# Performance work log

Measured on AMD Instinct MI355X. Metric: run time of the kernel, lower is better.

Reference implementation:

```python
import jax, jax.numpy as jnp
import numpy as np

N = 4096          # nodes
E = 131072        # edges (avg degree 32)
D_IN = 128        # node_dim
H = 256           # hidden_dim
HEADS = 8
DH = H // HEADS


def setup_inputs() -> dict:
    key = jax.random.key(0)
    ks = jax.random.split(key, 24)
    w = lambda k, shape: (jax.random.normal(k, shape, dtype=jnp.float32) * 0.05)
    inp = {
        "x": jax.random.normal(ks[0], (N, D_IN), dtype=jnp.float32),
        "edge_index": jax.random.randint(ks[1], (2, E), 0, N, dtype=jnp.int32),
        # GCN conv weights (PyG GCNConv: out = aggr(norm * x @ W) + b)
        "W1": w(ks[2], (D_IN, H)), "b1": jnp.zeros((H,), jnp.float32),
        "W2": w(ks[3], (H, H)),    "b2": jnp.zeros((H,), jnp.float32),
        "W3": w(ks[4], (H, H)),    "b3": jnp.zeros((H,), jnp.float32),
        # nn.MultiheadAttention params (torch layout: y = x @ W.T + b)
        "in_w": w(ks[5], (3 * H, H)), "in_b": jnp.zeros((3 * H,), jnp.float32),
        "out_w": w(ks[6], (H, H)),    "out_b": jnp.zeros((H,), jnp.float32),
        # failure_predictor MLP: H -> H/2 -> 3
        "fp1_w": w(ks[7], (H // 2, H)), "fp1_b": jnp.zeros((H // 2,), jnp.float32),
        "fp2_w": w(ks[8], (3, H // 2)), "fp2_b": jnp.zeros((3,), jnp.float32),
        # pattern_detector MLP: H -> H/2 -> 10
        "pd1_w": w(ks[9], (H // 2, H)),  "pd1_b": jnp.zeros((H // 2,), jnp.float32),
        "pd2_w": w(ks[10], (10, H // 2)), "pd2_b": jnp.zeros((10,), jnp.float32),
    }
    return inp


def gcn_conv(x, src, dst, W, b):
    """PyG GCNConv with self-loops and symmetric normalization."""
    h = x @ W                                   # [N, H]
    deg = jnp.zeros((N,), x.dtype).at[dst].add(1.0) + 1.0   # +1 for self-loop
    dinv = jax.lax.rsqrt(deg)
    norm = dinv[src] * dinv[dst]                # [E]
    agg = jnp.zeros_like(h).at[dst].add(h[src] * norm[:, None])
    agg = agg + h * (1.0 / deg)[:, None]        # self-loop term: deg^-1/2 * deg^-1/2
    return agg + b


def mha(h, in_w, in_b, out_w, out_b):
    qkv = h @ in_w.T + in_b                     # [N, 3H]
    q, k, v = jnp.split(qkv, 3, axis=-1)
    q = q.reshape(N, HEADS, DH).transpose(1, 0, 2)   # [h, N, dh]
    k = k.reshape(N, HEADS, DH).transpose(1, 0, 2)
    v = v.reshape(N, HEADS, DH).transpose(1, 0, 2)
    scores = jnp.einsum("hnd,hmd->hnm", q, k) / np.sqrt(DH)
    attn = jax.nn.softmax(scores, axis=-1)
    o = jnp.einsum("hnm,hmd->hnd", attn, v)          # [h, N, dh]
    o = o.transpose(1, 0, 2).reshape(N, H)
    return o @ out_w.T + out_b


def reference(x, edge_index, W1, b1, W2, b2, W3, b3, in_w, in_b, out_w, out_b,
              fp1_w, fp1_b, fp2_w, fp2_b, pd1_w, pd1_b, pd2_w, pd2_b):
    src, dst = edge_index[0], edge_index[1]
    h = jax.nn.relu(gcn_conv(x, src, dst, W1, b1))   # dropout is identity in eval
    h = jax.nn.relu(gcn_conv(h, src, dst, W2, b2))
    h = gcn_conv(h, src, dst, W3, b3)
    h = h + mha(h, in_w, in_b, out_w, out_b)
    risk = jax.nn.softmax(jax.nn.relu(h @ fp1_w.T + fp1_b) @ fp2_w.T + fp2_b, axis=-1)
    patterns = jax.nn.sigmoid(jax.nn.relu(h @ pd1_w.T + pd1_b) @ pd2_w.T + pd2_b)
    return risk, patterns
```

## Files before the change

### kernel.cpp

```cpp
#include <hip/hip_runtime.h>
#include <math.h>

static constexpr int NNODE = 4096;
static constexpr int HDIM  = 256;
static constexpr int DIN   = 128;
static constexpr int HEADS = 8;
static constexpr int SPLIT = 4;

using short8 = __attribute__((ext_vector_type(8))) short;
using f32x4  = __attribute__((ext_vector_type(4))) float;

__device__ inline unsigned short bfr(float x) {
    union { float f; unsigned u; } v; v.f = x;
    unsigned r = v.u + 0x7FFFu + ((v.u >> 16) & 1u);
    return (unsigned short)(r >> 16);
}
__device__ inline float bf2f(unsigned short u) {
    union { unsigned u; float f; } v; v.u = (unsigned)u << 16; return v.f;
}
__device__ inline unsigned cvt_pk_bf16(float lo, float hi) {
    unsigned r;
    asm("v_cvt_pk_bf16_f32 %0, %1, %2" : "=v"(r) : "v"(lo), "v"(hi));
    return r;
}
__device__ inline float ex2(float x) {
    float r;
    asm("v_exp_f32 %0, %1" : "=v"(r) : "v"(x));
    return r;
}

static constexpr float QSCALE_LOG2 = 0.25503527f;

__global__ __launch_bounds__(256) void k_scan_norm(const int* __restrict__ degi,
        int* __restrict__ off, int* __restrict__ cursor,
        float* __restrict__ dinv, float* __restrict__ invdeg) {
    __shared__ int partial[256];
    int t = threadIdx.x;
    int local[16];
    int s = 0;
    #pragma unroll
    for (int i = 0; i < 16; ++i) { local[i] = degi[t * 16 + i]; s += local[i]; }
    partial[t] = s;
    __syncthreads();
    #pragma unroll
    for (int d = 1; d < 256; d <<= 1) {
        int add = (t >= d) ? partial[t - d] : 0;
        __syncthreads();
        partial[t] += add;
        __syncthreads();
    }
    int b = partial[t] - s;
    #pragma unroll
    for (int i = 0; i < 16; ++i) {
        int n = t * 16 + i;
        off[n] = b; cursor[n] = b; b += local[i];
        float d = (float)local[i] + 1.0f;
        dinv[n]   = rsqrtf(d);
        invdeg[n] = 1.0f / d;
    }
}

__global__ void k_fill(const int* __restrict__ ei, int* __restrict__ cursor,
                       int* __restrict__ csr, int E) {
    int e = blockIdx.x * 256 + threadIdx.x;
    if (e < E) {
        int d = ei[E + e];
        int p = atomicAdd(&cursor[d], 1);
        csr[p] = ei[e];
    }
}

__global__ __launch_bounds__(256) void k_prep(
        const float* __restrict__ W1, const float* __restrict__ W2,
        const float* __restrict__ W3, const float* __restrict__ in_w,
        const float* __restrict__ outw, const float* __restrict__ fp1w,
        const float* __restrict__ pd1w, const float* __restrict__ fp1b,
        const float* __restrict__ pd1b, const float* __restrict__ x,
        const int* __restrict__ ei, int E, int* __restrict__ degi,
        unsigned short* __restrict__ W1t, unsigned short* __restrict__ W2t,
        unsigned short* __restrict__ W3t, unsigned short* __restrict__ in_wb,
        unsigned short* __restrict__ outwb, unsigned short* __restrict__ wcatb,
        float* __restrict__ bcat, unsigned short* __restrict__ xb) {
    int idx = blockIdx.x * 256 + threadIdx.x;
    if (idx < 32768) {
        int c = idx >> 7, k = idx & 127;
        W1t[idx] = bfr(W1[(size_t)k * 256 + c]);
    } else if (idx < 98304) {
        int j = idx - 32768; int c = j >> 8, k = j & 255;
        W2t[j] = bfr(W2[(size_t)k * 256 + c]);
    } else if (idx < 163840) {
        int j = idx - 98304; int c = j >> 8, k = j & 255;
        W3t[j] = bfr(W3[(size_t)k * 256 + c]);
    } else if (idx < 360448) {
        int j = idx - 163840;
        in_wb[j] = bfr(in_w[j]);
    } else if (idx < 425984) {
        int j = idx - 360448;
        outwb[j] = bfr(outw[j]);
    } else if (idx < 491520) {
        int j = idx - 425984;
        int row = j >> 8, k = j & 255;
        wcatb[j] = bfr(row < 128 ? fp1w[(size_t)row * 256 + k]
                                 : pd1w[(size_t)(row - 128) * 256 + k]);
        if (j < 256) bcat[j] = (j < 128) ? fp1b[j] : pd1b[j - 128];
    } else if (idx < 557056) {
        int i = (idx - 491520) * 8;
        float4 a = *(const float4*)&x[i];
        float4 b = *(const float4*)&x[i + 4];
        short8 o;
        o[0]=(short)bfr(a.x); o[1]=(short)bfr(a.y); o[2]=(short)bfr(a.z); o[3]=(short)bfr(a.w);
        o[4]=(short)bfr(b.x); o[5]=(short)bfr(b.y); o[6]=(short)bfr(b.z); o[7]=(short)bfr(b.w);
        *(short8*)&xb[i] = o;
    } else if (idx < 557056 + E) {
        atomicAdd(&degi[ei[E + (idx - 557056)]], 1);
    }
}

template<int K, int EPI, bool BIAS, bool ADD>
__global__ __launch_bounds__(256) void k_bgemm(
        const unsigned short* __restrict__ A, const unsigned short* __restrict__ B,
        const float* __restrict__ bias, const float* __restrict__ addsrc,
        void* __restrict__ P0, void* __restrict__ P1, void* __restrict__ P2,
        int Nout) {
    const int lane = threadIdx.x & 63, wave = threadIdx.x >> 6;
    const int ql = lane & 15, g = lane >> 4;
    const int m0w = blockIdx.y * 64 + wave * 16;
    const int n0 = blockIdx.x * 32;
    const unsigned short* ap = A + (size_t)(m0w + ql) * K + g * 8;
    const unsigned short* bp = B + (size_t)(n0 + ql) * K + g * 8;

    f32x4 acc[2] = {{0,0,0,0},{0,0,0,0}};
    #pragma unroll
    for (int k0 = 0; k0 < K; k0 += 32) {
        short8 a = *(const short8*)(ap + k0);
        #pragma unroll
        for (int nt = 0; nt < 2; ++nt) {
            short8 b = *(const short8*)(bp + (size_t)nt * 16 * K + k0);
            acc[nt] = __builtin_amdgcn_mfma_f32_16x16x32_bf16(a, b, acc[nt], 0, 0, 0);
        }
    }
    #pragma unroll
    for (int nt = 0; nt < 2; ++nt) {
        const int col = n0 + nt * 16 + ql;
        const float bv = BIAS ? bias[col] : 0.f;
        if (EPI == 2) {
            const int sec = col >> 8, cc = col & 255;
            const int head = cc >> 5, dh = cc & 31;
            if (sec == 2) {
                unsigned short* dst = (unsigned short*)P2
                    + ((size_t)head * 32 + dh) * NNODE + m0w + g * 4;
                uint2 pk;
                pk.x = cvt_pk_bf16(acc[nt][0] + bv, acc[nt][1] + bv);
                pk.y = cvt_pk_bf16(acc[nt][2] + bv, acc[nt][3] + bv);
                *(uint2*)dst = pk;
            } else {
                unsigned short* dst = (unsigned short*)(sec == 0 ? P0 : P1);
                const float sc = (sec == 0) ? QSCALE_LOG2 : 1.0f;
                #pragma unroll
                for (int i = 0; i < 4; ++i) {
                    int row = m0w + g * 4 + i;
                    dst[((size_t)head * NNODE + row) * 32 + dh] = bfr((acc[nt][i] + bv) * sc);
                }
            }
        } else if (EPI == 1) {
            unsigned short* Cb = (unsigned short*)P0;
            #pragma unroll
            for (int i = 0; i < 4; ++i) {
                int row = m0w + g * 4 + i;
                float v = acc[nt][i] + bv;
                if (ADD) v += addsrc[(size_t)row * Nout + col];
                Cb[(size_t)row * Nout + col] = bfr(v);
            }
        } else {
            float* Cf = (float*)P0;
            #pragma unroll
            for (int i = 0; i < 4; ++i) {
                int row = m0w + g * 4 + i;
                float v = acc[nt][i] + bv;
                if (ADD) v += addsrc[(size_t)row * Nout + col];
                Cf[(size_t)row * Nout + col] = v;
            }
        }
    }
}

__global__ __launch_bounds__(256) void k_bgemm_merge(
        const unsigned short* __restrict__ po, const float* __restrict__ pl,
        const unsigned short* __restrict__ B, const float* __restrict__ bias,
        const float* __restrict__ addsrc, unsigned short* __restrict__ Cb) {
    constexpr int K = HDIM;
    const int lane = threadIdx.x & 63, wave = threadIdx.x >> 6;
    const int ql = lane & 15, g = lane >> 4;
    const int m0w = blockIdx.y * 64 + wave * 16;
    const int n0 = blockIdx.x * 32;
    const int row = m0w + ql;
    const unsigned short* bp = B + (size_t)(n0 + ql) * K + g * 8;

    f32x4 acc[2] = {{0,0,0,0},{0,0,0,0}};
    #pragma unroll
    for (int k0 = 0; k0 < K; k0 += 32) {
        const int kidx = k0 + g * 8;
        const int hd = kidx >> 5, dh0 = kidx & 31;
        const size_t b4 = ((size_t)hd * NNODE + row) * SPLIT;
        float L = pl[b4] + pl[b4 + 1] + pl[b4 + 2] + pl[b4 + 3];
        float rcpL = 1.f / L;
        short8 p0 = *(const short8*)&po[(b4 + 0) * 32 + dh0];
        short8 p1 = *(const short8*)&po[(b4 + 1) * 32 + dh0];
        short8 p2 = *(const short8*)&po[(b4 + 2) * 32 + dh0];
        short8 p3 = *(const short8*)&po[(b4 + 3) * 32 + dh0];
        float vch[8];
        #pragma unroll
        for (int i = 0; i < 8; ++i) {
            vch[i] = (bf2f((unsigned short)p0[i]) + bf2f((unsigned short)p1[i])
                    + bf2f((unsigned short)p2[i]) + bf2f((unsigned short)p3[i])) * rcpL;
        }
        short8 a;
        #pragma unroll
        for (int i = 0; i < 4; ++i) {
            unsigned pk = cvt_pk_bf16(vch[2*i], vch[2*i+1]);
            a[2*i]   = (short)(pk & 0xFFFF);
            a[2*i+1] = (short)(pk >> 16);
        }
        #pragma unroll
        for (int nt = 0; nt < 2; ++nt) {
            short8 b = *(const short8*)(bp + (size_t)nt * 16 * K + k0);
            acc[nt] = __builtin_amdgcn_mfma_f32_16x16x32_bf16(a, b, acc[nt], 0, 0, 0);
        }
    }
    #pragma unroll
    for (int nt = 0; nt < 2; ++nt) {
        const int col = n0 + nt * 16 + ql;
        const float bv = bias[col];
        #pragma unroll
        for (int i = 0; i < 4; ++i) {
            int r = m0w + g * 4 + i;
            float v = acc[nt][i] + bv + addsrc[(size_t)r * HDIM + col];
            Cb[(size_t)r * HDIM + col] = bfr(v);
        }
    }
}

template<int MODE>
__global__ __launch_bounds__(256) void k_gather(const unsigned short* __restrict__ hW,
        const int* __restrict__ csr, const int* __restrict__ off,
        const int* __restrict__ degi, const float* __restrict__ dinv,
        const float* __restrict__ invdeg, const float* __restrict__ bias,
        float* __restrict__ aggf, unsigned short* __restrict__ aggb) {
    const int n = blockIdx.x;
    const int c = threadIdx.x;
    const int start = off[n];
    const int cnt = degi[n];
    __shared__ int   sidx[64];
    __shared__ float swht[64];
    float a0 = 0.f, a1 = 0.f, a2 = 0.f, a3 = 0.f;
    for (int k0 = 0; k0 < cnt; k0 += 64) {
        __syncthreads();
        if (c < 64 && k0 + c < cnt) {
            int s = csr[start + k0 + c];
            sidx[c] = s;
            swht[c] = dinv[s];
        }
        __syncthreads();
        int lim = min(64, cnt - k0);
        int k = 0;
        for (; k + 4 <= lim; k += 4) {
            a0 += bf2f(hW[(size_t)sidx[k+0] * HDIM + c]) * swht[k+0];
            a1 += bf2f(hW[(size_t)sidx[k+1] * HDIM + c]) * swht[k+1];
            a2 += bf2f(hW[(size_t)sidx[k+2] * HDIM + c]) * swht[k+2];
            a3 += bf2f(hW[(size_t)sidx[k+3] * HDIM + c]) * swht[k+3];
        }
        for (; k < lim; ++k)
            a0 += bf2f(hW[(size_t)sidx[k] * HDIM + c]) * swht[k];
    }
    float acc = (a0 + a1) + (a2 + a3);
    float val = acc * dinv[n] + bf2f(hW[(size_t)n * HDIM + c]) * invdeg[n] + bias[c];
    if (MODE == 0) {
        aggb[(size_t)n * HDIM + c] = bfr(fmaxf(val, 0.f));
    } else {
        aggf[(size_t)n * HDIM + c] = val;
        aggb[(size_t)n * HDIM + c] = bfr(val);
    }
}

__device__ inline void softmax_16q(f32x4 st[4], float& l,
        unsigned short* prow, int g) {
    float ll = 0.f;
    #pragma unroll
    for (int t = 0; t < 4; ++t) {
        float p0 = ex2(st[t][0]);
        float p1 = ex2(st[t][1]);
        float p2 = ex2(st[t][2]);
        float p3 = ex2(st[t][3]);
        ll += (p0 + p1) + (p2 + p3);
        uint2 w2; w2.x = cvt_pk_bf16(p0, p1); w2.y = cvt_pk_bf16(p2, p3);
        *(uint2*)&prow[t * 16 + g * 4] = w2;
    }
    ll += __shfl_xor(ll, 16);
    ll += __shfl_xor(ll, 32);
    l += ll;
}

__global__ __launch_bounds__(256, 4) void k_attn_mfma(const unsigned short* __restrict__ qh,
        const unsigned short* __restrict__ kh, const unsigned short* __restrict__ vt,
        unsigned short* __restrict__ po, float* __restrict__ pl) {
    const int bid = blockIdx.x;
    const int hd = bid & 7;
    const int z  = (bid >> 3) & (SPLIT - 1);
    const int qb = bid >> 5;
    const int tid = threadIdx.x;
    const int wave = tid >> 6, lane = tid & 63;
    const int ql = lane & 15, g = lane >> 4;

    __shared__ unsigned short Klds[2][64 * 40];
    __shared__ unsigned short Vt[2][32 * 72];
    __shared__ unsigned short Plds[4][16 * 72];

    const unsigned short* khh = kh + (size_t)hd * NNODE * 32;
    const unsigned short* vtt = vt + (size_t)hd * 32 * NNODE;
    const int row = qb * 64 + wave * 16 + ql;
    short8 qf = *(const short8*)(qh + ((size_t)hd * NNODE + row) * 32 + g * 8);

    f32x4 oa0 = {0,0,0,0}, oa1 = {0,0,0,0};
    float l = 0.f;

    const int skey = tid >> 2, skc = (tid & 3) * 8;
    const int sdh = tid >> 3, sch = (tid & 7) * 8;
    const unsigned short* ksrc = khh + (size_t)skey * 32 + skc;
    const unsigned short* vsrc = vtt + (size_t)sdh * NNODE + sch;
    unsigned short* prow = &Plds[wave][ql * 72];
    const int TPS = NNODE / 64 / SPLIT;
    const int t0 = z * TPS;

    {
        short8 kv = *(const short8*)(ksrc + (size_t)t0 * 64 * 32);
        short8 vv = *(const short8*)(vsrc + t0 * 64);
        *(short8*)&Klds[0][skey * 40 + skc] = kv;
        *(short8*)&Vt[0][sdh * 72 + sch] = vv;
    }
    __syncthreads();
    int cur = 0;

    for (int kt = t0; kt < t0 + TPS; ++kt) {
        short8 kv, vv;
        const bool pref = (kt + 1 < t0 + TPS);
        if (pref) {
            kv = *(const short8*)(ksrc + (size_t)(kt + 1) * 64 * 32);
            vv = *(const short8*)(vsrc + (kt + 1) * 64);
        }

        f32x4 st[4];
        __builtin_amdgcn_s_setprio(1);
        #pragma unroll
        for (int t = 0; t < 4; ++t) {
            short8 kf = *(const short8*)&Klds[cur][(t * 16 + ql) * 40 + g * 8];
            st[t] = __builtin_amdgcn_mfma_f32_16x16x32_bf16(kf, qf, (f32x4){0,0,0,0}, 0, 0, 0);
        }
        __builtin_amdgcn_s_setprio(0);

        softmax_16q(st, l, prow, g);

        if (pref) {
            *(short8*)&Klds[cur ^ 1][skey * 40 + skc] = kv;
            *(short8*)&Vt[cur ^ 1][sdh * 72 + sch] = vv;
        }

        __builtin_amdgcn_s_setprio(1);
        #pragma unroll
        for (int c = 0; c < 2; ++c) {
            short8 pf = *(const short8*)&prow[c * 32 + g * 8];
            short8 v0 = *(const short8*)&Vt[cur][ql * 72 + c * 32 + g * 8];
            short8 v1 = *(const short8*)&Vt[cur][(16 + ql) * 72 + c * 32 + g * 8];
            oa0 = __builtin_amdgcn_mfma_f32_16x16x32_bf16(v0, pf, oa0, 0, 0, 0);
            oa1 = __builtin_amdgcn_mfma_f32_16x16x32_bf16(v1, pf, oa1, 0, 0, 0);
        }
        __builtin_amdgcn_s_setprio(0);

        __syncthreads();
        cur ^= 1;
    }

    const size_t pidx = ((size_t)hd * NNODE + row) * SPLIT + z;
    unsigned short* pp = po + pidx * 32;
    uint2 r;
    r.x = cvt_pk_bf16(oa0[0], oa0[1]); r.y = cvt_pk_bf16(oa0[2], oa0[3]);
    *(uint2*)&pp[g * 4] = r;
    r.x = cvt_pk_bf16(oa1[0], oa1[1]); r.y = cvt_pk_bf16(oa1[2], oa1[3]);
    *(uint2*)&pp[16 + g * 4] = r;
    if (g == 0) pl[pidx] = l;
}

__global__ __launch_bounds__(256) void k_heads2(const float* __restrict__ th,
        const float* __restrict__ fp2w, const float* __restrict__ fp2b,
        const float* __restrict__ pd2w, const float* __restrict__ pd2b,
        float* __restrict__ out) {
    const int wave = threadIdx.x >> 6, lane = threadIdx.x & 63;
    const int n = blockIdx.x * 4 + wave;
    const int half = lane >> 5;
    const int li = lane & 31;
    float4 h4 = *(const float4*)&th[(size_t)n * HDIM + half * 128 + li * 4];
    h4.x = fmaxf(h4.x, 0.f); h4.y = fmaxf(h4.y, 0.f);
    h4.z = fmaxf(h4.z, 0.f); h4.w = fmaxf(h4.w, 0.f);
    float lf[3];
    float lp[10];
    #pragma unroll
    for (int j = 0; j < 10; ++j) {
        float partial = 0.f;
        if (half == 0) {
            if (j < 3) {
                float4 wv = *(const float4*)&fp2w[j * 128 + li * 4];
                partial = h4.x*wv.x + h4.y*wv.y + h4.z*wv.z + h4.w*wv.w;
            }
        } else {
            float4 wv = *(const float4*)&pd2w[j * 128 + li * 4];
            partial = h4.x*wv.x + h4.y*wv.y + h4.z*wv.z + h4.w*wv.w;
        }
        #pragma unroll
        for (int d = 1; d < 32; d <<= 1) partial += __shfl_xor(partial, d);
        if (j < 3) lf[j] = partial;
        lp[j] = partial;
    }
    if (lane == 0) {
        float l0 = lf[0] + fp2b[0], l1 = lf[1] + fp2b[1], l2 = lf[2] + fp2b[2];
        float mx = fmaxf(l0, fmaxf(l1, l2));
        float e0 = __expf(l0 - mx), e1 = __expf(l1 - mx), e2 = __expf(l2 - mx);
        float inv = 1.f / (e0 + e1 + e2);
        out[(size_t)n * 3 + 0] = e0 * inv;
        out[(size_t)n * 3 + 1] = e1 * inv;
        out[(size_t)n * 3 + 2] = e2 * inv;
    } else if (lane == 32) {
        #pragma unroll
        for (int j = 0; j < 10; ++j)
            out[(size_t)NNODE * 3 + (size_t)n * 10 + j] =
                1.f / (1.f + __expf(-(lp[j] + pd2b[j])));
    }
}

extern "C" void kernel_launch(void* const* d_in, const int* in_sizes, int n_in,
                              void* d_out, int out_size, void* d_ws, size_t ws_size,
                              hipStream_t stream) {
    const float* x    = (const float*)d_in[0];
    const int*   ei   = (const int*)  d_in[1];
    const float* W1   = (const float*)d_in[2];
    const float* b1   = (const float*)d_in[3];
    const float* W2   = (const float*)d_in[4];
    const float* b2   = (const float*)d_in[5];
    const float* W3   = (const float*)d_in[6];
    const float* b3   = (const float*)d_in[7];
    const float* in_w = (const float*)d_in[8];
    const float* in_b = (const float*)d_in[9];
    const float* outw = (const float*)d_in[10];
    const float* outb = (const float*)d_in[11];
    const float* fp1w = (const float*)d_in[12];
    const float* fp1b = (const float*)d_in[13];
    const float* fp2w = (const float*)d_in[14];
    const float* fp2b = (const float*)d_in[15];
    const float* pd1w = (const float*)d_in[16];
    const float* pd1b = (const float*)d_in[17];
    const float* pd2w = (const float*)d_in[18];
    const float* pd2b = (const float*)d_in[19];
    float* out = (float*)d_out;

    const int E = in_sizes[1] / 2;

    char* w = (char*)d_ws;
    auto alloc = [&](size_t bytes) {
        char* p = w; w += (bytes + 255) & ~(size_t)255; return p;
    };
    int*   degi   = (int*)alloc(NNODE * 4);
    int*   off    = (int*)alloc(NNODE * 4);
    int*   cursor = (int*)alloc(NNODE * 4);
    int*   csr    = (int*)alloc((size_t)E * 4);
    float* dinv   = (float*)alloc(NNODE * 4);
    float* invdeg = (float*)alloc(NNODE * 4);
    unsigned short* W1t   = (unsigned short*)alloc(256 * 128 * 2);
    unsigned short* W2t   = (unsigned short*)alloc(256 * 256 * 2);
    unsigned short* W3t   = (unsigned short*)alloc(256 * 256 * 2);
    unsigned short* in_wb = (unsigned short*)alloc(768 * 256 * 2);
    unsigned short* outwb = (unsigned short*)alloc(256 * 256 * 2);
    unsigned short* wcatb = (unsigned short*)alloc(256 * 256 * 2);
    float* bcat  = (float*)alloc(256 * 4);
    unsigned short* xb    = (unsigned short*)alloc((size_t)NNODE * DIN * 2);
    float* bufA  = (float*)alloc((size_t)NNODE * HDIM * 4);
    unsigned short* bufAb = (unsigned short*)alloc((size_t)NNODE * HDIM * 2);
    unsigned short* aggb1 = (unsigned short*)alloc((size_t)NNODE * HDIM * 2);
    unsigned short* aggb2 = (unsigned short*)alloc((size_t)NNODE * HDIM * 2);
    float* hf    = (float*)alloc((size_t)NNODE * HDIM * 4);
    unsigned short* hb    = (unsigned short*)alloc((size_t)NNODE * HDIM * 2);
    unsigned short* qh    = (unsigned short*)alloc((size_t)HEADS * NNODE * 32 * 2);
    unsigned short* kh    = (unsigned short*)alloc((size_t)HEADS * NNODE * 32 * 2);
    unsigned short* vt    = (unsigned short*)alloc((size_t)HEADS * 32 * NNODE * 2);
    unsigned short* po    = (unsigned short*)alloc((size_t)HEADS * NNODE * SPLIT * 32 * 2);
    float* pl    = (float*)alloc((size_t)HEADS * NNODE * SPLIT * 4);
    unsigned short* hfinb = (unsigned short*)alloc((size_t)NNODE * HDIM * 2);

    hipMemsetAsync(degi, 0, NNODE * sizeof(int), stream);
    const int prep_slots = 557056 + E;
    k_prep<<<(prep_slots + 255) / 256, 256, 0, stream>>>(
        W1, W2, W3, in_w, outw, fp1w, pd1w, fp1b, pd1b, x, ei, E, degi,
        W1t, W2t, W3t, in_wb, outwb, wcatb, bcat, xb);
    k_scan_norm<<<1, 256, 0, stream>>>(degi, off, cursor, dinv, invdeg);
    k_fill<<<(E + 255) / 256, 256, 0, stream>>>(ei, cursor, csr, E);

    dim3 g256(HDIM / 32, NNODE / 64);
    dim3 g768(768 / 32, NNODE / 64);

    k_bgemm<DIN, 1, false, false><<<g256, 256, 0, stream>>>(xb, W1t, nullptr, nullptr, bufAb, nullptr, nullptr, HDIM);
    k_gather<0><<<NNODE, 256, 0, stream>>>(bufAb, csr, off, degi, dinv, invdeg, b1, nullptr, aggb1);
    k_bgemm<HDIM, 1, false, false><<<g256, 256, 0, stream>>>(aggb1, W2t, nullptr, nullptr, bufAb, nullptr, nullptr, HDIM);
    k_gather<0><<<NNODE, 256, 0, stream>>>(bufAb, csr, off, degi, dinv, invdeg, b2, nullptr, aggb2);
    k_bgemm<HDIM, 1, false, false><<<g256, 256, 0, stream>>>(aggb2, W3t, nullptr, nullptr, bufAb, nullptr, nullptr, HDIM);
    k_gather<1><<<NNODE, 256, 0, stream>>>(bufAb, csr, off, degi, dinv, invdeg, b3, hf, hb);

    k_bgemm<HDIM, 2, true, false><<<g768, 256, 0, stream>>>(hb, in_wb, in_b, nullptr, qh, kh, vt, 768);
    k_attn_mfma<<<HEADS * SPLIT * (NNODE / 64), 256, 0, stream>>>(qh, kh, vt, po, pl);
    k_bgemm_merge<<<g256, 256, 0, stream>>>(po, pl, outwb, outb, hf, hfinb);

    k_bgemm<HDIM, 0, true, false><<<g256, 256, 0, stream>>>(hfinb, wcatb, bcat, nullptr, bufA, nullptr, nullptr, HDIM);
    k_heads2<<<NNODE / 4, 256, 0, stream>>>(bufA, fp2w, fp2b, pd2w, pd2b, out);
}
```

Baseline: 185.9 us.

## Aggregate before transform in GCN layers and use wave-per-node vectorized gather

Uses associativity (A·X)·W = A·(X·W) to aggregate neighbor features first and apply the weight matrix afterwards. Bias and ReLU move into the GEMM epilogue, and the first layer now gathers 128-wide input rows instead of 256-wide ones. The gather kernel is rewritten so each wave handles one node, broadcasts neighbor indices with shuffles instead of shared memory and block barriers, and loads 2 or 4 packed bf16 values per lane. A new epilogue writes both the fp32 and bf16 outputs of the last layer. The trade-off is that aggregated values are rounded to bf16 before the GEMM, which slightly changes numerics.

After: 189.9 us. 2.2% more time.

```diff
diff --git a/kernel.cpp b/kernel.cpp
--- a/kernel.cpp
+++ b/kernel.cpp
@@ -17,6 +17,12 @@
 }
 __device__ inline float bf2f(unsigned short u) {
     union { unsigned u; float f; } v; v.u = (unsigned)u << 16; return v.f;
+}
+__device__ inline float bf2f_lo(unsigned u) {
+    union { unsigned u; float f; } v; v.u = u << 16; return v.f;
+}
+__device__ inline float bf2f_hi(unsigned u) {
+    union { unsigned u; float f; } v; v.u = u & 0xFFFF0000u; return v.f;
 }
 __device__ inline unsigned cvt_pk_bf16(float lo, float hi) {
     unsigned r;
@@ -116,6 +122,59 @@
     }
 }
 
+template<int CHL>
+__global__ __launch_bounds__(256) void k_gather2(const unsigned short* __restrict__ hW,
+        const int* __restrict__ csr, const int* __restrict__ off,
+        const int* __restrict__ degi, const float* __restrict__ dinv,
+        const float* __restrict__ invdeg, unsigned short* __restrict__ aggb) {
+    constexpr int CH = 64 * CHL;
+    const int wave = threadIdx.x >> 6, lane = threadIdx.x & 63;
+    const int n = blockIdx.x * 4 + wave;
+    const int start = off[n];
+    const int cnt = degi[n];
+    float a0 = 0.f, a1 = 0.f, a2 = 0.f, a3 = 0.f;
+    for (int k0 = 0; k0 < cnt; k0 += 64) {
+        int myidx = 0; float myw = 0.f;
+        if (k0 + lane < cnt) {
+            myidx = csr[start + k0 + lane];
+            myw = dinv[myidx];
+        }
+        int lim = min(64, cnt - k0);
+        for (int k = 0; k < lim; ++k) {
+            int s = __shfl(myidx, k);
+            float wgt = __shfl(myw, k);
+            if (CHL == 4) {
+                uint2 hv = *(const uint2*)&hW[(size_t)s * CH + lane * 4];
+                a0 += bf2f_lo(hv.x) * wgt;
+                a1 += bf2f_hi(hv.x) * wgt;
+                a2 += bf2f_lo(hv.y) * wgt;
+                a3 += bf2f_hi(hv.y) * wgt;
+            } else {
+                unsigned hv = *(const unsigned*)&hW[(size_t)s * CH + lane * 2];
+                a0 += bf2f_lo(hv) * wgt;
+                a1 += bf2f_hi(hv) * wgt;
+            }
+        }
+    }
+    float dn = dinv[n], idg = invdeg[n];
+    if (CHL == 4) {
+        uint2 sv = *(const uint2*)&hW[(size_t)n * CH + lane * 4];
+        float v0 = a0 * dn + bf2f_lo(sv.x) * idg;
+        float v1 = a1 * dn + bf2f_hi(sv.x) * idg;
+        float v2 = a2 * dn + bf2f_lo(sv.y) * idg;
+        float v3 = a3 * dn + bf2f_hi(sv.y) * idg;
+        uint2 pk;
+        pk.x = cvt_pk_bf16(v0, v1);
+        pk.y = cvt_pk_bf16(v2, v3);
+        *(uint2*)&aggb[(size_t)n * CH + lane * 4] = pk;
+    } else {
+        unsigned sv = *(const unsigned*)&hW[(size_t)n * CH + lane * 2];
+        float v0 = a0 * dn + bf2f_lo(sv) * idg;
+        float v1 = a1 * dn + bf2f_hi(sv) * idg;
+        *(unsigned*)&aggb[(size_t)n * CH + lane * 2] = cvt_pk_bf16(v0, v1);
+    }
+}
+
 template<int K, int EPI, bool BIAS, bool ADD>
 __global__ __launch_bounds__(256) void k_bgemm(
         const unsigned short* __restrict__ A, const unsigned short* __restrict__ B,
@@ -162,14 +221,25 @@
                     dst[((size_t)head * NNODE + row) * 32 + dh] = bfr((acc[nt][i] + bv) * sc);
                 }
             }
-        } else if (EPI == 1) {
+        } else if (EPI == 1 || EPI == 3) {
             unsigned short* Cb = (unsigned short*)P0;
             #pragma unroll
             for (int i = 0; i < 4; ++i) {
                 int row = m0w + g * 4 + i;
                 float v = acc[nt][i] + bv;
                 if (ADD) v += addsrc[(size_t)row * Nout + col];
+                if (EPI == 3) v = fmaxf(v, 0.f);
                 Cb[(size_t)row * Nout + col] = bfr(v);
+            }
+        } else if (EPI == 4) {
+            unsigned short* Cb = (unsigned short*)P0;
+            float* Cf = (float*)P1;
+            #pragma unroll
+            for (int i = 0; i < 4; ++i) {
+                int row = m0w + g * 4 + i;
+                float v = acc[nt][i] + bv;
+                Cb[(size_t)row * Nout + col] = bfr(v);
+                Cf[(size_t)row * Nout + col] = v;
             }
         } else {
             float* Cf = (float*)P0;
@@ -237,48 +307,6 @@
             float v = acc[nt][i] + bv + addsrc[(size_t)r * HDIM + col];
             Cb[(size_t)r * HDIM + col] = bfr(v);
         }
-    }
-}
-
-template<int MODE>
-__global__ __launch_bounds__(256) void k_gather(const unsigned short* __restrict__ hW,
-        const int* __restrict__ csr, const int* __restrict__ off,
-        const int* __restrict__ degi, const float* __restrict__ dinv,
-        const float* __restrict__ invdeg, const float* __restrict__ bias,
-        float* __restrict__ aggf, unsigned short* __restrict__ aggb) {
-    const int n = blockIdx.x;
-    const int c = threadIdx.x;
-    const int start = off[n];
-    const int cnt = degi[n];
-    __shared__ int   sidx[64];
-    __shared__ float swht[64];
-    float a0 = 0.f, a1 = 0.f, a2 = 0.f, a3 = 0.f;
-    for (int k0 = 0; k0 < cnt; k0 += 64) {
-        __syncthreads();
-        if (c < 64 && k0 + c < cnt) {
-            int s = csr[start + k0 + c];
-            sidx[c] = s;
-            swht[c] = dinv[s];
-        }
-        __syncthreads();
-        int lim = min(64, cnt - k0);
-        int k = 0;
-        for (; k + 4 <= lim; k += 4) {
-            a0 += bf2f(hW[(size_t)sidx[k+0] * HDIM + c]) * swht[k+0];
-            a1 += bf2f(hW[(size_t)sidx[k+1] * HDIM + c]) * swht[k+1];
-            a2 += bf2f(hW[(size_t)sidx[k+2] * HDIM + c]) * swht[k+2];
-            a3 += bf2f(hW[(size_t)sidx[k+3] * HDIM + c]) * swht[k+3];
-        }
-        for (; k < lim; ++k)
-            a0 += bf2f(hW[(size_t)sidx[k] * HDIM + c]) * swht[k];
-    }
-    float acc = (a0 + a1) + (a2 + a3);
-    float val = acc * dinv[n] + bf2f(hW[(size_t)n * HDIM + c]) * invdeg[n] + bias[c];
-    if (MODE == 0) {
-        aggb[(size_t)n * HDIM + c] = bfr(fmaxf(val, 0.f));
-    } else {
-        aggf[(size_t)n * HDIM + c] = val;
-        aggb[(size_t)n * HDIM + c] = bfr(val);
     }
 }
 
@@ -480,10 +508,12 @@
     unsigned short* wcatb = (unsigned short*)alloc(256 * 256 * 2);
     float* bcat  = (float*)alloc(256 * 4);
     unsigned short* xb    = (unsigned short*)alloc((size_t)NNODE * DIN * 2);
+    unsigned short* g1b   = (unsigned short*)alloc((size_t)NNODE * DIN * 2);
     float* bufA  = (float*)alloc((size_t)NNODE * HDIM * 4);
-    unsigned short* bufAb = (unsigned short*)alloc((size_t)NNODE * HDIM * 2);
-    unsigned short* aggb1 = (unsigned short*)alloc((size_t)NNODE * HDIM * 2);
-    unsigned short* aggb2 = (unsigned short*)alloc((size_t)NNODE * HDIM * 2);
+    unsigned short* h1b   = (unsigned short*)alloc((size_t)NNODE * HDIM * 2);
+    unsigned short* g2b   = (unsigned short*)alloc((size_t)NNODE * HDIM * 2);
+    unsigned short* h2b   = (unsigned short*)alloc((size_t)NNODE * HDIM * 2);
+    unsigned short* g3b   = (unsigned short*)alloc((size_t)NNODE * HDIM * 2);
     float* hf    = (float*)alloc((size_t)NNODE * HDIM * 4);
     unsigned short* hb    = (unsigned short*)alloc((size_t)NNODE * HDIM * 2);
     unsigned short* qh    = (unsigned short*)alloc((size_t)HEADS * NNODE * 32 * 2);
@@ -504,12 +534,12 @@
     dim3 g256(HDIM / 32, NNODE / 64);
     dim3 g768(768 / 32, NNODE / 64);
 
-    k_bgemm<DIN, 1, false, false><<<g256, 256, 0, stream>>>(xb, W1t, nullptr, nullptr, bufAb, nullptr, nullptr, HDIM);
-    k_gather<0><<<NNODE, 256, 0, stream>>>(bufAb, csr, off, degi, dinv, invdeg, b1, nullptr, aggb1);
-    k_bgemm<HDIM, 1, false, false><<<g256, 256, 0, stream>>>(aggb1, W2t, nullptr, nullptr, bufAb, nullptr, nullptr, HDIM);
-    k_gather<0><<<NNODE, 256, 0, stream>>>(bufAb, csr, off, degi, dinv, invdeg, b2, nullptr, aggb2);
-    k_bgemm<HDIM, 1, false, false><<<g256, 256, 0, stream>>>(aggb2, W3t, nullptr, nullptr, bufAb, nullptr, nullptr, HDIM);
-    k_gather<1><<<NNODE, 256, 0, stream>>>(bufAb, csr, off, degi, dinv, invdeg, b3, hf, hb);
+    k_gather2<2><<<NNODE / 4, 256, 0, stream>>>(xb, csr, off, degi, dinv, invdeg, g1b);
+    k_bgemm<DIN, 3, true, false><<<g256, 256, 0, stream>>>(g1b, W1t, b1, nullptr, h1b, nullptr, nullptr, HDIM);
+    k_gather2<4><<<NNODE / 4, 256, 0, stream>>>(h1b, csr, off, degi, dinv, invdeg, g2b);
+    k_bgemm<HDIM, 3, true, false><<<g256, 256, 0, stream>>>(g2b, W2t, b2, nullptr, h2b, nullptr, nullptr, HDIM);
+    k_gather2<4><<<NNODE / 4, 256, 0, stream>>>(h2b, csr, off, degi, dinv, invdeg, g3b);
+    k_bgemm<HDIM, 4, true, false><<<g256, 256, 0, stream>>>(g3b, W3t, b3, nullptr, hb, hf, nullptr, HDIM);
 
     k_bgemm<HDIM, 2, true, false><<<g768, 256, 0, stream>>>(hb, in_wb, in_b, nullptr, qh, kh, vt, 768);
     k_attn_mfma<<<HEADS * SPLIT * (NNODE / 64), 256, 0, stream>>>(qh, kh, vt, po, pl);
```
